# Kernel tuning notes

Hardware: AMD Instinct MI355X
Metric: run time of the kernel (lower is better)

The kernel has to match this reference:

```python
import jax, jax.numpy as jnp
import numpy as np

WINDOW = 7
SHIFT = 3
HEADS = 4


def _rel_pos_index(w):
    # same construction as ShiftedWindowAttention.__init__ (numpy, static)
    coords = np.stack(np.meshgrid(np.arange(w), np.arange(w), indexing='ij'))  # [2,w,w]
    cf = coords.reshape(2, -1)                       # [2, w*w]
    rc = (cf[:, :, None] - cf[:, None, :]).transpose(1, 2, 0)  # [L,L,2]
    rc[:, :, 0] += w - 1
    rc[:, :, 1] += w - 1
    rc[:, :, 0] *= 2 * w - 1
    return rc.sum(-1).reshape(-1)                    # [L*L]


def _attn_mask(H, W, w, s):
    # cyclic-shift attention mask, static numpy constant
    m = np.zeros((H, W))
    slices = ((0, -w), (-w, -s), (-s, None))
    cnt = 0
    for hs in slices:
        for ws in slices:
            m[hs[0]:hs[1], ws[0]:ws[1]] = cnt
            cnt += 1
    m = m.reshape(H // w, w, W // w, w).transpose(0, 2, 1, 3).reshape(-1, w * w)  # [nwin, L]
    d = m[:, None, :] - m[:, :, None]                # [nwin, L, L]
    return np.where(d != 0, -100.0, 0.0).astype(np.float32)


def setup_inputs() -> dict:
    key = jax.random.key(0)
    ks = jax.random.split(key, 6)
    B, H, W, C = 64, 56, 56, 128
    return {
        'x': jax.random.normal(ks[0], (B, H, W, C), dtype=jnp.float32),
        'qkv_weight': jax.random.normal(ks[1], (3 * C, C), dtype=jnp.float32) * 0.02,
        'qkv_bias': jax.random.normal(ks[2], (3 * C,), dtype=jnp.float32) * 0.02,
        'proj_weight': jax.random.normal(ks[3], (C, C), dtype=jnp.float32) * 0.02,
        'proj_bias': jax.random.normal(ks[4], (C,), dtype=jnp.float32) * 0.02,
        'rel_bias_table': jax.random.normal(ks[5], ((2 * WINDOW - 1) ** 2, HEADS), dtype=jnp.float32) * 0.02,
    }


def reference(x, qkv_weight, qkv_bias, proj_weight, proj_bias, rel_bias_table):
    B, H, W, C = x.shape
    w, s, h = WINDOW, SHIFT, HEADS
    d = C // h
    nH, nW = H // w, W // w
    nwin = nH * nW
    L = w * w

    # relative position bias: [h, L, L]
    bias = rel_bias_table[jnp.asarray(_rel_pos_index(w))].reshape(L, L, h).transpose(2, 0, 1)

    # cyclic shift + window partition -> [B*nwin, L, C]
    xs = jnp.roll(x, (-s, -s), axis=(1, 2))
    xw = xs.reshape(B, nH, w, nW, w, C).transpose(0, 1, 3, 2, 4, 5).reshape(B * nwin, L, C)

    # fused qkv projection (F.linear: x @ W.T + b)
    qkv = (xw @ qkv_weight.T + qkv_bias).reshape(B * nwin, L, 3, h, d).transpose(2, 0, 3, 1, 4)
    q, k, v = qkv[0] * (d ** -0.5), qkv[1], qkv[2]   # each [B*nwin, h, L, d]

    attn = jnp.einsum('nhqd,nhkd->nhqk', q, k) + bias[None]
    mask = jnp.asarray(_attn_mask(H, W, w, s))       # [nwin, L, L]
    attn = attn.reshape(B, nwin, h, L, L) + mask[None, :, None]
    attn = jax.nn.softmax(attn.reshape(B * nwin, h, L, L), axis=-1)

    out = jnp.einsum('nhqk,nhkd->nhqd', attn, v).transpose(0, 2, 1, 3).reshape(B * nwin, L, C)
    out = out @ proj_weight.T + proj_bias

    # window merge + reverse shift -> [B, H, W, C]
    out = out.reshape(B, nH, nW, w, w, C).transpose(0, 1, 3, 2, 4, 5).reshape(B, H, W, C)
    return jnp.roll(out, (s, s), axis=(1, 2))
```

## Files before the change

### kernel.cpp

```cpp
#include <hip/hip_runtime.h>

typedef __attribute__((ext_vector_type(8))) short short8;
typedef __attribute__((ext_vector_type(4))) float f32x4;

static __device__ __forceinline__ unsigned short f2bf(float f) {
  union { float f; unsigned int u; } v; v.f = f;
  unsigned int r = v.u + 0x7FFFu + ((v.u >> 16) & 1u);
  return (unsigned short)(r >> 16);
}
static __device__ __forceinline__ unsigned int pack2(float a, float b) {
  return (unsigned int)f2bf(a) | ((unsigned int)f2bf(b) << 16);
}

#define QO 0
#define KO 2560
#define VO 5120
#define TO 7424
#define WSTRIDE 7776

__global__ __launch_bounds__(256) void k_prep(const float* __restrict__ wq,
    const float* __restrict__ wp, unsigned short* __restrict__ dq,
    unsigned short* __restrict__ dp) {
  int i = blockIdx.x * 256 + threadIdx.x;
  if (i < 384 * 128) dq[i] = f2bf(wq[i]);
  if (i < 128 * 128) dp[i] = f2bf(wp[i]);
}

static __device__ __forceinline__ int reg3(int y) { return y < 49 ? 0 : (y < 53 ? 1 : 2); }

__global__ __launch_bounds__(256, 2) void k_fused(const float* __restrict__ x,
    const unsigned short* __restrict__ Wq, const float* __restrict__ qb,
    const unsigned short* __restrict__ Wp, const float* __restrict__ pb,
    const float* __restrict__ table, float* __restrict__ out) {
  __shared__ __align__(16) unsigned short lds[4 * WSTRIDE];
  const int tid = threadIdx.x;
  const int win = blockIdx.x;
  const int b = win >> 6, wl = win & 63;
  const int wh = wl >> 3, ww = wl & 7;
  const int wv = tid >> 6, ln = tid & 63;
  const int l15 = ln & 15, l4 = ln >> 4;
  unsigned short* W = lds + wv * WSTRIDE;
  float* tblw = (float*)&W[TO];

  for (int i = ln; i < 169; i += 64) tblw[i] = table[i * 4 + wv];

  const float* rp[4];
  bool vld[4];
#pragma unroll
  for (int mt = 0; mt < 4; ++mt) {
    const int t = mt * 16 + l15;
    vld[mt] = (t < 49);
    const int tc = vld[mt] ? t : 0;
    const int th = tc / 7, tw = tc - th * 7;
    int sh = wh * 7 + th + 3; if (sh >= 56) sh -= 56;
    int sw = ww * 7 + tw + 3; if (sw >= 56) sw -= 56;
    rp[mt] = x + (((size_t)(b * 56 + sh)) * 56 + sw) * 128;
  }
  int nrow[6];
#pragma unroll
  for (int j = 0; j < 6; ++j)
    nrow[j] = (j >> 1) * 128 + wv * 32 + (j & 1) * 16 + l15;

  const f32x4 z4 = {0.f, 0.f, 0.f, 0.f};
  f32x4 aS[4][4], aV[4][2];
#pragma unroll
  for (int mt = 0; mt < 4; ++mt) {
#pragma unroll
    for (int j = 0; j < 4; ++j) aS[mt][j] = z4;
#pragma unroll
    for (int j = 0; j < 2; ++j) aV[mt][j] = z4;
  }
#pragma unroll
  for (int ks = 0; ks < 4; ++ks) {
    short8 af[4], bf[6];
#pragma unroll
    for (int mt = 0; mt < 4; ++mt) {
      const float4* p = (const float4*)(rp[mt] + ks * 32 + l4 * 8);
      float4 fa = p[0], fb = p[1];
      uint4 u;
      u.x = pack2(fa.x, fa.y); u.y = pack2(fa.z, fa.w);
      u.z = pack2(fb.x, fb.y); u.w = pack2(fb.z, fb.w);
      u.x = vld[mt] ? u.x : 0u; u.y = vld[mt] ? u.y : 0u;
      u.z = vld[mt] ? u.z : 0u; u.w = vld[mt] ? u.w : 0u;
      af[mt] = *(short8*)&u;
    }
#pragma unroll
    for (int j = 0; j < 6; ++j)
      bf[j] = *(const short8*)&Wq[(size_t)nrow[j] * 128 + ks * 32 + l4 * 8];
#pragma unroll
    for (int mt = 0; mt < 4; ++mt) {
#pragma unroll
      for (int j = 0; j < 4; ++j)
        aS[mt][j] = __builtin_amdgcn_mfma_f32_16x16x32_bf16(bf[j], af[mt], aS[mt][j], 0, 0, 0);
#pragma unroll
      for (int j = 0; j < 2; ++j)
        aV[mt][j] = __builtin_amdgcn_mfma_f32_16x16x32_bf16(af[mt], bf[4 + j], aV[mt][j], 0, 0, 0);
    }
  }
  {
    const float SC = 0.17677669529663687f;
    const float4 bq0 = *(const float4*)(qb + wv * 32 + 4 * l4);
    const float4 bq1 = *(const float4*)(qb + wv * 32 + 16 + 4 * l4);
    const float4 bk0 = *(const float4*)(qb + 128 + wv * 32 + 4 * l4);
    const float4 bk1 = *(const float4*)(qb + 128 + wv * 32 + 16 + 4 * l4);
    const float bv0 = qb[256 + wv * 32 + l15];
    const float bv1 = qb[256 + wv * 32 + 16 + l15];
#pragma unroll
    for (int mt = 0; mt < 4; ++mt) {
      const int t = mt * 16 + l15;
      uint2 u;
      u.x = pack2((aS[mt][0][0] + bq0.x) * SC, (aS[mt][0][1] + bq0.y) * SC);
      u.y = pack2((aS[mt][0][2] + bq0.z) * SC, (aS[mt][0][3] + bq0.w) * SC);
      *(uint2*)&W[QO + t * 40 + 4 * l4] = u;
      u.x = pack2((aS[mt][1][0] + bq1.x) * SC, (aS[mt][1][1] + bq1.y) * SC);
      u.y = pack2((aS[mt][1][2] + bq1.z) * SC, (aS[mt][1][3] + bq1.w) * SC);
      *(uint2*)&W[QO + t * 40 + 16 + 4 * l4] = u;
      u.x = pack2(aS[mt][2][0] + bk0.x, aS[mt][2][1] + bk0.y);
      u.y = pack2(aS[mt][2][2] + bk0.z, aS[mt][2][3] + bk0.w);
      *(uint2*)&W[KO + t * 40 + 4 * l4] = u;
      u.x = pack2(aS[mt][3][0] + bk1.x, aS[mt][3][1] + bk1.y);
      u.y = pack2(aS[mt][3][2] + bk1.z, aS[mt][3][3] + bk1.w);
      *(uint2*)&W[KO + t * 40 + 16 + 4 * l4] = u;
      u.x = pack2(aV[mt][0][0] + bv0, aV[mt][0][1] + bv0);
      u.y = pack2(aV[mt][0][2] + bv0, aV[mt][0][3] + bv0);
      *(uint2*)&W[VO + l15 * 72 + mt * 16 + 4 * l4] = u;
      u.x = pack2(aV[mt][1][0] + bv1, aV[mt][1][1] + bv1);
      u.y = pack2(aV[mt][1][2] + bv1, aV[mt][1][3] + bv1);
      *(uint2*)&W[VO + (16 + l15) * 72 + mt * 16 + 4 * l4] = u;
    }
  }

  f32x4 s[4][4];
#pragma unroll
  for (int mt = 0; mt < 4; ++mt)
#pragma unroll
    for (int nt = 0; nt < 4; ++nt) s[mt][nt] = z4;
  {
    short8 qf[4], kf[4];
#pragma unroll
    for (int mt = 0; mt < 4; ++mt)
      qf[mt] = *(const short8*)&W[QO + (mt * 16 + l15) * 40 + l4 * 8];
#pragma unroll
    for (int nt = 0; nt < 4; ++nt)
      kf[nt] = *(const short8*)&W[KO + (nt * 16 + l15) * 40 + l4 * 8];
#pragma unroll
    for (int mt = 0; mt < 4; ++mt)
#pragma unroll
      for (int nt = 0; nt < 4; ++nt)
        s[mt][nt] = __builtin_amdgcn_mfma_f32_16x16x32_bf16(kf[nt], qf[mt], s[mt][nt], 0, 0, 0);
  }

  int ih4[4], iw4[4], irg[4];
#pragma unroll
  for (int mt = 0; mt < 4; ++mt) {
    const int i = mt * 16 + l15;
    const int ihh = i / 7, iww = i - ihh * 7;
    ih4[mt] = ihh; iw4[mt] = iww;
    irg[mt] = 3 * reg3(wh * 7 + ihh) + reg3(ww * 7 + iww);
  }
  float pmax[4] = {-1e30f, -1e30f, -1e30f, -1e30f};
#pragma unroll
  for (int nt = 0; nt < 4; ++nt) {
#pragma unroll
    for (int r = 0; r < 4; ++r) {
      const int j = nt * 16 + 4 * l4 + r;
      const int jhh = j / 7, jww = j - jhh * 7;
      const int jrg = 3 * reg3(wh * 7 + jhh) + reg3(ww * 7 + jww);
      const bool jbad = (j >= 49);
#pragma unroll
      for (int mt = 0; mt < 4; ++mt) {
        int didx = (ih4[mt] - jhh + 6) * 13 + (iw4[mt] - jww + 6);
        didx = didx < 0 ? 0 : (didx > 168 ? 168 : didx);
        float v = s[mt][nt][r] + tblw[didx];
        if (irg[mt] != jrg) v -= 100.0f;
        if (jbad) v = -1e30f;
        s[mt][nt][r] = v;
        pmax[mt] = fmaxf(pmax[mt], v);
      }
    }
  }
  float inv[4];
#pragma unroll
  for (int mt = 0; mt < 4; ++mt) {
    float m0 = pmax[mt];
    m0 = fmaxf(m0, __shfl_xor(m0, 16));
    m0 = fmaxf(m0, __shfl_xor(m0, 32));
    float sum = 0.0f;
#pragma unroll
    for (int nt = 0; nt < 4; ++nt)
#pragma unroll
      for (int r = 0; r < 4; ++r) {
        const float v = s[mt][nt][r];
        const float e = (v > -1e29f) ? __expf(v - m0) : 0.0f;
        s[mt][nt][r] = e;
        sum += e;
      }
    sum += __shfl_xor(sum, 16);
    sum += __shfl_xor(sum, 32);
    inv[mt] = 1.0f / sum;
  }

  f32x4 o[4][2];
#pragma unroll
  for (int mt = 0; mt < 4; ++mt)
#pragma unroll
    for (int dt = 0; dt < 2; ++dt) o[mt][dt] = z4;
#pragma unroll
  for (int mt = 0; mt < 4; ++mt) {
    const int i = mt * 16 + l15;
    if (i < 49) {
#pragma unroll
      for (int nt = 0; nt < 2; ++nt) {
        uint2 u;
        u.x = pack2(s[mt][nt][0] * inv[mt], s[mt][nt][1] * inv[mt]);
        u.y = pack2(s[mt][nt][2] * inv[mt], s[mt][nt][3] * inv[mt]);
        *(uint2*)&W[QO + i * 40 + nt * 16 + 4 * l4] = u;
      }
    }
  }
  {
    short8 pa[4], vb[2];
#pragma unroll
    for (int mt = 0; mt < 4; ++mt)
      pa[mt] = *(const short8*)&W[QO + (mt * 16 + l15) * 40 + l4 * 8];
#pragma unroll
    for (int dt = 0; dt < 2; ++dt)
      vb[dt] = *(const short8*)&W[VO + (dt * 16 + l15) * 72 + l4 * 8];
#pragma unroll
    for (int mt = 0; mt < 4; ++mt)
#pragma unroll
      for (int dt = 0; dt < 2; ++dt)
        o[mt][dt] = __builtin_amdgcn_mfma_f32_16x16x32_bf16(vb[dt], pa[mt], o[mt][dt], 0, 0, 0);
  }
#pragma unroll
  for (int mt = 0; mt < 4; ++mt) {
    const int i = mt * 16 + l15;
    if (i < 49) {
#pragma unroll
      for (int nt = 2; nt < 4; ++nt) {
        uint2 u;
        u.x = pack2(s[mt][nt][0] * inv[mt], s[mt][nt][1] * inv[mt]);
        u.y = pack2(s[mt][nt][2] * inv[mt], s[mt][nt][3] * inv[mt]);
        *(uint2*)&W[QO + i * 40 + (nt - 2) * 16 + 4 * l4] = u;
      }
    }
  }
  {
    short8 pa[4], vb[2];
#pragma unroll
    for (int mt = 0; mt < 4; ++mt)
      pa[mt] = *(const short8*)&W[QO + (mt * 16 + l15) * 40 + l4 * 8];
#pragma unroll
    for (int dt = 0; dt < 2; ++dt)
      vb[dt] = *(const short8*)&W[VO + (dt * 16 + l15) * 72 + 32 + l4 * 8];
#pragma unroll
    for (int mt = 0; mt < 4; ++mt)
#pragma unroll
      for (int dt = 0; dt < 2; ++dt)
        o[mt][dt] = __builtin_amdgcn_mfma_f32_16x16x32_bf16(vb[dt], pa[mt], o[mt][dt], 0, 0, 0);
  }
#pragma unroll
  for (int mt = 0; mt < 4; ++mt) {
    const int t = mt * 16 + l15;
#pragma unroll
    for (int dt = 0; dt < 2; ++dt) {
      uint2 u;
      u.x = pack2(o[mt][dt][0], o[mt][dt][1]);
      u.y = pack2(o[mt][dt][2], o[mt][dt][3]);
      *(uint2*)&W[KO + t * 40 + dt * 16 + 4 * l4] = u;
    }
  }
  __syncthreads();

  const float4 pbv0 = *(const float4*)(pb + wv * 32 + 4 * l4);
  const float4 pbv1 = *(const float4*)(pb + wv * 32 + 16 + 4 * l4);
  f32x4 c2[4][2];
#pragma unroll
  for (int mt = 0; mt < 4; ++mt)
#pragma unroll
    for (int nt = 0; nt < 2; ++nt) c2[mt][nt] = z4;
#pragma unroll
  for (int ks = 0; ks < 4; ++ks) {
    short8 a2[4], bp[2];
#pragma unroll
    for (int mt = 0; mt < 4; ++mt)
      a2[mt] = *(const short8*)&lds[ks * WSTRIDE + KO + (mt * 16 + l15) * 40 + l4 * 8];
#pragma unroll
    for (int nt = 0; nt < 2; ++nt)
      bp[nt] = *(const short8*)&Wp[(size_t)(wv * 32 + nt * 16 + l15) * 128 + ks * 32 + l4 * 8];
#pragma unroll
    for (int mt = 0; mt < 4; ++mt)
#pragma unroll
      for (int nt = 0; nt < 2; ++nt)
        c2[mt][nt] = __builtin_amdgcn_mfma_f32_16x16x32_bf16(bp[nt], a2[mt], c2[mt][nt], 0, 0, 0);
  }
#pragma unroll
  for (int mt = 0; mt < 4; ++mt) {
    const int t = mt * 16 + l15;
    if (t < 49) {
      const int th = t / 7, tw = t - th * 7;
      int y = wh * 7 + th + 3; if (y >= 56) y -= 56;
      int xx = ww * 7 + tw + 3; if (xx >= 56) xx -= 56;
      float* dstp = out + (((size_t)(b * 56 + y)) * 56 + xx) * 128 + wv * 32 + 4 * l4;
      float4 v0, v1;
      v0.x = c2[mt][0][0] + pbv0.x; v0.y = c2[mt][0][1] + pbv0.y;
      v0.z = c2[mt][0][2] + pbv0.z; v0.w = c2[mt][0][3] + pbv0.w;
      *(float4*)(dstp) = v0;
      v1.x = c2[mt][1][0] + pbv1.x; v1.y = c2[mt][1][1] + pbv1.y;
      v1.z = c2[mt][1][2] + pbv1.z; v1.w = c2[mt][1][3] + pbv1.w;
      *(float4*)(dstp + 16) = v1;
    }
  }
}

extern "C" void kernel_launch(void* const* d_in, const int* in_sizes, int n_in,
                              void* d_out, int out_size, void* d_ws, size_t ws_size,
                              hipStream_t stream) {
  const float* x     = (const float*)d_in[0];
  const float* qkvw  = (const float*)d_in[1];
  const float* qkvb  = (const float*)d_in[2];
  const float* projw = (const float*)d_in[3];
  const float* projb = (const float*)d_in[4];
  const float* table = (const float*)d_in[5];
  float* out = (float*)d_out;
  char* ws = (char*)d_ws;
  unsigned short* Wq = (unsigned short*)ws;
  unsigned short* Wp = (unsigned short*)(ws + 98304);

  k_prep<<<dim3(192), dim3(256), 0, stream>>>(qkvw, projw, Wq, Wp);
  k_fused<<<dim3(4096), dim3(256), 0, stream>>>(x, Wq, qkvb, Wp, projb, table, out);
}
```

Measured before the change: 154.0 us.

## Precompute combined bias/mask tables and shrink LDS to raise occupancy

The prep kernel now builds four variants (edge or interior window in each axis) of the per-head relative-position-bias-plus-shift-mask matrix, padded to 64x64. The fused kernel loads these with vector reads instead of computing region ids and table indices per element. The V tile is written to LDS after the QK^T matmul so it can reuse the K buffer, which shrinks per-wave LDS and allows launch bounds of 3 blocks per CU. The trade is an extra 256KB bias read through cache per window and a larger prep kernel.

After: 169.5 us. 1.1x slower.

```diff
diff --git a/kernel.cpp b/kernel.cpp
--- a/kernel.cpp
+++ b/kernel.cpp
@@ -12,37 +12,46 @@
   return (unsigned int)f2bf(a) | ((unsigned int)f2bf(b) << 16);
 }
 
-#define QO 0
-#define KO 2560
-#define VO 5120
-#define TO 7424
-#define WSTRIDE 7776
+#define B1 0
+#define B2 2560
+#define WS2 5120
 
 __global__ __launch_bounds__(256) void k_prep(const float* __restrict__ wq,
-    const float* __restrict__ wp, unsigned short* __restrict__ dq,
-    unsigned short* __restrict__ dp) {
-  int i = blockIdx.x * 256 + threadIdx.x;
-  if (i < 384 * 128) dq[i] = f2bf(wq[i]);
-  if (i < 128 * 128) dp[i] = f2bf(wp[i]);
-}
-
-static __device__ __forceinline__ int reg3(int y) { return y < 49 ? 0 : (y < 53 ? 1 : 2); }
-
-__global__ __launch_bounds__(256, 2) void k_fused(const float* __restrict__ x,
+    const float* __restrict__ wp, const float* __restrict__ tbl,
+    unsigned short* __restrict__ dq, unsigned short* __restrict__ dp,
+    float* __restrict__ biasM) {
+  const int n = blockIdx.x * 256 + threadIdx.x;
+  if (n < 384 * 128) dq[n] = f2bf(wq[n]);
+  if (n < 128 * 128) dp[n] = f2bf(wp[n]);
+  if (n < 65536) {
+    const int j = n & 63, i = (n >> 6) & 63;
+    const int h = (n >> 12) & 3, bb = (n >> 14) & 1, aa = (n >> 15) & 1;
+    float val;
+    if (i >= 49) val = 0.0f;
+    else if (j >= 49) val = -1e30f;
+    else {
+      const int ih = i / 7, iw = i - ih * 7, jh = j / 7, jw = j - jh * 7;
+      const int didx = (ih - jh + 6) * 13 + (iw - jw + 6);
+      const int irg = (aa ? (ih < 4 ? 3 : 6) : 0) + (bb ? (iw < 4 ? 1 : 2) : 0);
+      const int jrg = (aa ? (jh < 4 ? 3 : 6) : 0) + (bb ? (jw < 4 ? 1 : 2) : 0);
+      val = tbl[didx * 4 + h] - (irg != jrg ? 100.0f : 0.0f);
+    }
+    biasM[n] = val;
+  }
+}
+
+__global__ __launch_bounds__(256, 3) void k_fused(const float* __restrict__ x,
     const unsigned short* __restrict__ Wq, const float* __restrict__ qb,
     const unsigned short* __restrict__ Wp, const float* __restrict__ pb,
-    const float* __restrict__ table, float* __restrict__ out) {
-  __shared__ __align__(16) unsigned short lds[4 * WSTRIDE];
+    const float* __restrict__ biasM, float* __restrict__ out) {
+  __shared__ __align__(16) unsigned short lds[4 * WS2];
   const int tid = threadIdx.x;
   const int win = blockIdx.x;
   const int b = win >> 6, wl = win & 63;
   const int wh = wl >> 3, ww = wl & 7;
   const int wv = tid >> 6, ln = tid & 63;
   const int l15 = ln & 15, l4 = ln >> 4;
-  unsigned short* W = lds + wv * WSTRIDE;
-  float* tblw = (float*)&W[TO];
-
-  for (int i = ln; i < 169; i += 64) tblw[i] = table[i * 4 + wv];
+  unsigned short* W = lds + wv * WS2;
 
   const float* rp[4];
   bool vld[4];
@@ -103,77 +112,71 @@
     const float4 bq1 = *(const float4*)(qb + wv * 32 + 16 + 4 * l4);
     const float4 bk0 = *(const float4*)(qb + 128 + wv * 32 + 4 * l4);
     const float4 bk1 = *(const float4*)(qb + 128 + wv * 32 + 16 + 4 * l4);
-    const float bv0 = qb[256 + wv * 32 + l15];
-    const float bv1 = qb[256 + wv * 32 + 16 + l15];
 #pragma unroll
     for (int mt = 0; mt < 4; ++mt) {
       const int t = mt * 16 + l15;
       uint2 u;
       u.x = pack2((aS[mt][0][0] + bq0.x) * SC, (aS[mt][0][1] + bq0.y) * SC);
       u.y = pack2((aS[mt][0][2] + bq0.z) * SC, (aS[mt][0][3] + bq0.w) * SC);
-      *(uint2*)&W[QO + t * 40 + 4 * l4] = u;
+      *(uint2*)&W[B1 + t * 40 + 4 * l4] = u;
       u.x = pack2((aS[mt][1][0] + bq1.x) * SC, (aS[mt][1][1] + bq1.y) * SC);
       u.y = pack2((aS[mt][1][2] + bq1.z) * SC, (aS[mt][1][3] + bq1.w) * SC);
-      *(uint2*)&W[QO + t * 40 + 16 + 4 * l4] = u;
+      *(uint2*)&W[B1 + t * 40 + 16 + 4 * l4] = u;
       u.x = pack2(aS[mt][2][0] + bk0.x, aS[mt][2][1] + bk0.y);
       u.y = pack2(aS[mt][2][2] + bk0.z, aS[mt][2][3] + bk0.w);
-      *(uint2*)&W[KO + t * 40 + 4 * l4] = u;
+      *(uint2*)&W[B2 + t * 40 + 4 * l4] = u;
       u.x = pack2(aS[mt][3][0] + bk1.x, aS[mt][3][1] + bk1.y);
       u.y = pack2(aS[mt][3][2] + bk1.z, aS[mt][3][3] + bk1.w);
-      *(uint2*)&W[KO + t * 40 + 16 + 4 * l4] = u;
+      *(uint2*)&W[B2 + t * 40 + 16 + 4 * l4] = u;
+    }
+  }
+
+  f32x4 s[4][4];
+#pragma unroll
+  for (int mt = 0; mt < 4; ++mt)
+#pragma unroll
+    for (int nt = 0; nt < 4; ++nt) s[mt][nt] = z4;
+  {
+    short8 qf[4], kf[4];
+#pragma unroll
+    for (int mt = 0; mt < 4; ++mt)
+      qf[mt] = *(const short8*)&W[B1 + (mt * 16 + l15) * 40 + l4 * 8];
+#pragma unroll
+    for (int nt = 0; nt < 4; ++nt)
+      kf[nt] = *(const short8*)&W[B2 + (nt * 16 + l15) * 40 + l4 * 8];
+#pragma unroll
+    for (int mt = 0; mt < 4; ++mt)
+#pragma unroll
+      for (int nt = 0; nt < 4; ++nt)
+        s[mt][nt] = __builtin_amdgcn_mfma_f32_16x16x32_bf16(kf[nt], qf[mt], s[mt][nt], 0, 0, 0);
+  }
+  {
+    const float bv0 = qb[256 + wv * 32 + l15];
+    const float bv1 = qb[256 + wv * 32 + 16 + l15];
+#pragma unroll
+    for (int mt = 0; mt < 4; ++mt) {
+      uint2 u;
       u.x = pack2(aV[mt][0][0] + bv0, aV[mt][0][1] + bv0);
       u.y = pack2(aV[mt][0][2] + bv0, aV[mt][0][3] + bv0);
-      *(uint2*)&W[VO + l15 * 72 + mt * 16 + 4 * l4] = u;
+      *(uint2*)&W[B2 + l15 * 72 + mt * 16 + 4 * l4] = u;
       u.x = pack2(aV[mt][1][0] + bv1, aV[mt][1][1] + bv1);
       u.y = pack2(aV[mt][1][2] + bv1, aV[mt][1][3] + bv1);
-      *(uint2*)&W[VO + (16 + l15) * 72 + mt * 16 + 4 * l4] = u;
-    }
-  }
-
-  f32x4 s[4][4];
-#pragma unroll
-  for (int mt = 0; mt < 4; ++mt)
-#pragma unroll
-    for (int nt = 0; nt < 4; ++nt) s[mt][nt] = z4;
-  {
-    short8 qf[4], kf[4];
-#pragma unroll
-    for (int mt = 0; mt < 4; ++mt)
-      qf[mt] = *(const short8*)&W[QO + (mt * 16 + l15) * 40 + l4 * 8];
-#pragma unroll
-    for (int nt = 0; nt < 4; ++nt)
-      kf[nt] = *(const short8*)&W[KO + (nt * 16 + l15) * 40 + l4 * 8];
-#pragma unroll
-    for (int mt = 0; mt < 4; ++mt)
-#pragma unroll
-      for (int nt = 0; nt < 4; ++nt)
-        s[mt][nt] = __builtin_amdgcn_mfma_f32_16x16x32_bf16(kf[nt], qf[mt], s[mt][nt], 0, 0, 0);
-  }
-
-  int ih4[4], iw4[4], irg[4];
+      *(uint2*)&W[B2 + (16 + l15) * 72 + mt * 16 + 4 * l4] = u;
+    }
+  }
+
+  const float* bm = biasM + (((wh == 7 ? 2 : 0) + (ww == 7 ? 1 : 0)) * 4 + wv) * 4096;
+  float pmax[4] = {-1e30f, -1e30f, -1e30f, -1e30f};
 #pragma unroll
   for (int mt = 0; mt < 4; ++mt) {
     const int i = mt * 16 + l15;
-    const int ihh = i / 7, iww = i - ihh * 7;
-    ih4[mt] = ihh; iw4[mt] = iww;
-    irg[mt] = 3 * reg3(wh * 7 + ihh) + reg3(ww * 7 + iww);
-  }
-  float pmax[4] = {-1e30f, -1e30f, -1e30f, -1e30f};
-#pragma unroll
-  for (int nt = 0; nt < 4; ++nt) {
-#pragma unroll
-    for (int r = 0; r < 4; ++r) {
-      const int j = nt * 16 + 4 * l4 + r;
-      const int jhh = j / 7, jww = j - jhh * 7;
-      const int jrg = 3 * reg3(wh * 7 + jhh) + reg3(ww * 7 + jww);
-      const bool jbad = (j >= 49);
-#pragma unroll
-      for (int mt = 0; mt < 4; ++mt) {
-        int didx = (ih4[mt] - jhh + 6) * 13 + (iw4[mt] - jww + 6);
-        didx = didx < 0 ? 0 : (didx > 168 ? 168 : didx);
-        float v = s[mt][nt][r] + tblw[didx];
-        if (irg[mt] != jrg) v -= 100.0f;
-        if (jbad) v = -1e30f;
+    const float* bmr = bm + i * 64 + 4 * l4;
+#pragma unroll
+    for (int nt = 0; nt < 4; ++nt) {
+      const f32x4 bv = *(const f32x4*)(bmr + nt * 16);
+#pragma unroll
+      for (int r = 0; r < 4; ++r) {
+        const float v = s[mt][nt][r] + bv[r];
         s[mt][nt][r] = v;
         pmax[mt] = fmaxf(pmax[mt], v);
       }
@@ -214,7 +217,7 @@
         uint2 u;
         u.x = pack2(s[mt][nt][0] * inv[mt], s[mt][nt][1] * inv[mt]);
         u.y = pack2(s[mt][nt][2] * inv[mt], s[mt][nt][3] * inv[mt]);
-        *(uint2*)&W[QO + i * 40 + nt * 16 + 4 * l4] = u;
+        *(uint2*)&W[B1 + i * 40 + nt * 16 + 4 * l4] = u;
       }
     }
   }
@@ -222,10 +225,10 @@
     short8 pa[4], vb[2];
 #pragma unroll
     for (int mt = 0; mt < 4; ++mt)
-      pa[mt] = *(const short8*)&W[QO + (mt * 16 + l15) * 40 + l4 * 8];
+      pa[mt] = *(const short8*)&W[B1 + (mt * 16 + l15) * 40 + l4 * 8];
 #pragma unroll
     for (int dt = 0; dt < 2; ++dt)
-      vb[dt] = *(const short8*)&W[VO + (dt * 16 + l15) * 72 + l4 * 8];
+      vb[dt] = *(const short8*)&W[B2 + (dt * 16 + l15) * 72 + l4 * 8];
 #pragma unroll
     for (int mt = 0; mt < 4; ++mt)
 #pragma unroll
@@ -241,7 +244,7 @@
         uint2 u;
         u.x = pack2(s[mt][nt][0] * inv[mt], s[mt][nt][1] * inv[mt]);
         u.y = pack2(s[mt][nt][2] * inv[mt], s[mt][nt][3] * inv[mt]);
-        *(uint2*)&W[QO + i * 40 + (nt - 2) * 16 + 4 * l4] = u;
+        *(uint2*)&W[B1 + i * 40 + (nt - 2) * 16 + 4 * l4] = u;
       }
     }
   }
@@ -249,10 +252,10 @@
     short8 pa[4], vb[2];
 #pragma unroll
     for (int mt = 0; mt < 4; ++mt)
-      pa[mt] = *(const short8*)&W[QO + (mt * 16 + l15) * 40 + l4 * 8];
+      pa[mt] = *(const short8*)&W[B1 + (mt * 16 + l15) * 40 + l4 * 8];
 #pragma unroll
     for (int dt = 0; dt < 2; ++dt)
-      vb[dt] = *(const short8*)&W[VO + (dt * 16 + l15) * 72 + 32 + l4 * 8];
+      vb[dt] = *(const short8*)&W[B2 + (dt * 16 + l15) * 72 + 32 + l4 * 8];
 #pragma unroll
     for (int mt = 0; mt < 4; ++mt)
 #pragma unroll
@@ -267,7 +270,7 @@
       uint2 u;
       u.x = pack2(o[mt][dt][0], o[mt][dt][1]);
       u.y = pack2(o[mt][dt][2], o[mt][dt][3]);
-      *(uint2*)&W[KO + t * 40 + dt * 16 + 4 * l4] = u;
+      *(uint2*)&W[B1 + t * 40 + dt * 16 + 4 * l4] = u;
     }
   }
   __syncthreads();
@@ -284,7 +287,7 @@
     short8 a2[4], bp[2];
 #pragma unroll
     for (int mt = 0; mt < 4; ++mt)
-      a2[mt] = *(const short8*)&lds[ks * WSTRIDE + KO + (mt * 16 + l15) * 40 + l4 * 8];
+      a2[mt] = *(const short8*)&lds[ks * WS2 + B1 + (mt * 16 + l15) * 40 + l4 * 8];
 #pragma unroll
     for (int nt = 0; nt < 2; ++nt)
       bp[nt] = *(const short8*)&Wp[(size_t)(wv * 32 + nt * 16 + l15) * 128 + ks * 32 + l4 * 8];
@@ -326,7 +329,8 @@
   char* ws = (char*)d_ws;
   unsigned short* Wq = (unsigned short*)ws;
   unsigned short* Wp = (unsigned short*)(ws + 98304);
-
-  k_prep<<<dim3(192), dim3(256), 0, stream>>>(qkvw, projw, Wq, Wp);
-  k_fused<<<dim3(4096), dim3(256), 0, stream>>>(x, Wq, qkvb, Wp, projb, table, out);
-}
+  float* biasM = (float*)(ws + 131072);
+
+  k_prep<<<dim3(256), dim3(256), 0, stream>>>(qkvw, projw, table, Wq, Wp, biasM);
+  k_fused<<<dim3(4096), dim3(256), 0, stream>>>(x, Wq, qkvb, Wp, projb, biasM, out);
+}
```
